# Performance work log

Measured on AMD Instinct MI355X. Metric: run time of the kernel, lower is better.

## Reference

```python
import jax, jax.numpy as jnp
import numpy as np

D_MODEL = 1024
NUM_HEADS = 16
D_K = D_MODEL // NUM_HEADS


def setup_inputs() -> dict:
    key = jax.random.key(0)
    ks = jax.random.split(key, 5)
    s = 1.0 / np.sqrt(D_MODEL)  # xavier-ish scale
    x = jax.random.normal(ks[0], (2, 2048, D_MODEL), dtype=jnp.float32)
    Wq = jax.random.normal(ks[1], (D_MODEL, D_MODEL), dtype=jnp.float32) * s
    Wk = jax.random.normal(ks[2], (D_MODEL, D_MODEL), dtype=jnp.float32) * s
    Wv = jax.random.normal(ks[3], (D_MODEL, D_MODEL), dtype=jnp.float32) * s
    Wo = jax.random.normal(ks[4], (D_MODEL, D_MODEL), dtype=jnp.float32) * s
    z = jnp.zeros((D_MODEL,), dtype=jnp.float32)
    return {"x": x, "Wq": Wq, "bq": z, "Wk": Wk, "bk": z, "Wv": Wv, "bv": z, "Wo": Wo, "bo": z}


def reference(x, Wq, bq, Wk, bk, Wv, bv, Wo, bo):
    B, S, _ = x.shape
    # torch Linear: y = x @ W.T + b
    def split_heads(t):
        return t.reshape(B, S, NUM_HEADS, D_K).transpose(0, 2, 1, 3)  # [B,H,S,Dk]
    q = split_heads(x @ Wq.T + bq)
    k = split_heads(x @ Wk.T + bk)
    v = split_heads(x @ Wv.T + bv)
    scores = jnp.einsum('bhqd,bhkd->bhqk', q, k) / jnp.sqrt(jnp.float32(D_K))
    attn = jax.nn.softmax(scores, axis=-1)
    out = jnp.einsum('bhqk,bhkd->bhqd', attn, v)  # [B,H,S,Dk]
    out = out.transpose(0, 2, 1, 3).reshape(B, S, D_MODEL)
    return out @ Wo.T + bo
```

## Files before the change

kernel.cpp:

```cpp
#include <hip/hip_runtime.h>
#include <hip/hip_bf16.h>
#include <type_traits>


typedef __attribute__((ext_vector_type(4))) float f32x4;
typedef __attribute__((ext_vector_type(16))) float f32x16;
typedef __attribute__((ext_vector_type(8))) short s16x8;
typedef __attribute__((ext_vector_type(4))) unsigned int u32x4;

#define GLDS16(g, l)                                                       \
  __builtin_amdgcn_global_load_lds(                                        \
      (const __attribute__((address_space(1))) unsigned int*)(g),          \
      (__attribute__((address_space(3))) unsigned int*)(l), 16, 0, 0)

#define SCALE_Q 0.18033688011112042f

__device__ __forceinline__ unsigned short f2bf(float f) {
  unsigned int u = __builtin_bit_cast(unsigned int, f);
  u += 0x7fffu + ((u >> 16) & 1u);
  return (unsigned short)(u >> 16);
}

__device__ __forceinline__ unsigned int cvtpk_bf16(float lo, float hi) {
  unsigned int r;
  asm("v_cvt_pk_bf16_f32 %0, %1, %2" : "=v"(r) : "v"(lo), "v"(hi));
  return r;
}

__device__ __forceinline__ float fexp2(float x) {
  return __builtin_amdgcn_exp2f(x);
}

__global__ void cvt_f32_bf16(const float* __restrict__ in,
                             unsigned short* __restrict__ out, int n,
                             float scale) {
  int i = (blockIdx.x * blockDim.x + threadIdx.x) * 4;
  if (i < n) {
    float4 v = *reinterpret_cast<const float4*>(in + i);
    ushort4 o;
    o.x = f2bf(v.x * scale); o.y = f2bf(v.y * scale);
    o.z = f2bf(v.z * scale); o.w = f2bf(v.w * scale);
    *reinterpret_cast<ushort4*>(out + i) = o;
  }
}

__global__ void concat3(const float* __restrict__ a, const float* __restrict__ b,
                        const float* __restrict__ c, float* __restrict__ out) {
  int i = blockIdx.x * blockDim.x + threadIdx.x;
  const float* src = (i < 1024) ? a : ((i < 2048) ? b : c);
  float s = (i < 1024) ? SCALE_Q : 1.0f;
  out[i] = src[i & 1023] * s;
}

template <typename CT>
__global__ __launch_bounds__(256, 2) void gemm_bt(
    const unsigned short* __restrict__ A, const unsigned short* __restrict__ B,
    CT* __restrict__ C, int M, int N, int K, const float* __restrict__ bias) {
  __shared__ unsigned short As[128 * 32];
  __shared__ unsigned short Bs[128 * 32];
  const int tid = threadIdx.x;
  const int wv = tid >> 6, lane = tid & 63;
  const int g = lane >> 4, c16 = lane & 15;
  const int wm = wv >> 1, wn = wv & 1;
  const int bm = blockIdx.y, bn = blockIdx.x;

  const unsigned short* Ab = A + (size_t)bm * 128 * K;
  const unsigned short* Bb = B + (size_t)bn * 128 * K;

  f32x4 acc[4][4] = {};

  for (int k0 = 0; k0 < K; k0 += 32) {
    __syncthreads();
#pragma unroll
    for (int r = 0; r < 2; ++r) {
      int i = r * 256 + tid;
      int row = i >> 2, col = (i & 3) * 8;
      GLDS16(Ab + (size_t)row * K + k0 + col, &As[i * 8]);
    }
#pragma unroll
    for (int r = 0; r < 2; ++r) {
      int i = r * 256 + tid;
      int row = i >> 2, col = (i & 3) * 8;
      GLDS16(Bb + (size_t)row * K + k0 + col, &Bs[i * 8]);
    }
    __syncthreads();

    s16x8 af[4], bfv[4];
#pragma unroll
    for (int m = 0; m < 4; ++m)
      af[m] = *(const s16x8*)&As[(wm * 64 + m * 16 + c16) * 32 + g * 8];
#pragma unroll
    for (int n = 0; n < 4; ++n)
      bfv[n] = *(const s16x8*)&Bs[(wn * 64 + n * 16 + c16) * 32 + g * 8];
#pragma unroll
    for (int m = 0; m < 4; ++m)
#pragma unroll
      for (int n = 0; n < 4; ++n)
        acc[m][n] = __builtin_amdgcn_mfma_f32_16x16x32_bf16(af[m], bfv[n],
                                                            acc[m][n], 0, 0, 0);
  }

#pragma unroll
  for (int m = 0; m < 4; ++m) {
#pragma unroll
    for (int n = 0; n < 4; ++n) {
      int col = bn * 128 + wn * 64 + n * 16 + c16;
      float bb = bias ? bias[col] : 0.f;
#pragma unroll
      for (int j = 0; j < 4; ++j) {
        int row = bm * 128 + wm * 64 + m * 16 + g * 4 + j;
        float v = acc[m][n][j] + bb;
        if constexpr (std::is_same<CT, float>::value)
          C[(size_t)row * N + col] = v;
        else
          C[(size_t)row * N + col] = f2bf(v);
      }
    }
  }
}

__global__ void transpose_v(const unsigned short* __restrict__ qkv,
                            unsigned short* __restrict__ vt) {
  __shared__ unsigned short T[64 * 80];
  const int tid = threadIdx.x;
  const int st = blockIdx.x, bh = blockIdx.y;
  const int b = bh >> 4, h = bh & 15;
  const int s0 = st * 64;

  int srow = tid >> 2, d0 = (tid & 3) * 16;
  const unsigned short* src =
      qkv + (size_t)(b * 2048 + s0 + srow) * 3072 + 2048 + h * 64 + d0;
  s16x8 v0 = *(const s16x8*)(src);
  s16x8 v1 = *(const s16x8*)(src + 8);
  *(s16x8*)&T[srow * 80 + d0] = v0;
  *(s16x8*)&T[srow * 80 + d0 + 8] = v1;
  __syncthreads();

  int drow = tid >> 2, sl = (tid & 3) * 16;
  s16x8 o0, o1;
#pragma unroll
  for (int j = 0; j < 8; ++j) o0[j] = (short)T[(sl + j) * 80 + drow];
#pragma unroll
  for (int j = 0; j < 8; ++j) o1[j] = (short)T[(sl + 8 + j) * 80 + drow];
  unsigned short* dst = vt + (size_t)(bh * 64 + drow) * 2048 + s0 + sl;
  *(s16x8*)dst = o0;
  *(s16x8*)(dst + 8) = o1;
}

__global__ __launch_bounds__(1024) void flash_attn(
    const unsigned short* __restrict__ qkv, const unsigned short* __restrict__ vt,
    unsigned short* __restrict__ attn) {
  __shared__ __align__(16) char smem[68608];
  unsigned short* KsB = (unsigned short*)smem;
  unsigned short* VTsB = (unsigned short*)(smem + 32768);
  float* MoB = (float*)smem;
  float* MlB = (float*)(smem + 66560);

  const int tid = threadIdx.x;
  const int wv = tid >> 6, lane = tid & 63;
  const int half = wv >> 3, w8 = wv & 7;
  const int col = lane & 31, hi = lane >> 5;
  const int qt = blockIdx.x, bh = blockIdx.y;
  const int b = bh >> 4, h = bh & 15;
  const int qrow0 = qt * 256 + w8 * 32;

  const int stid = tid & 511;
  const int srow = stid >> 3, scs = stid & 7;
  const int sqc = scs ^ (srow & 7);
  const int kbase = half * 1024;
  const unsigned short* kgsrc =
      qkv + (size_t)(b * 2048 + kbase + srow) * 3072 + 1024 + h * 64 + sqc * 8;
  const unsigned short* vgsrc =
      vt + (size_t)(bh * 64 + srow) * 2048 + kbase + sqc * 8;

  s16x8 qb[4];
#pragma unroll
  for (int ds = 0; ds < 4; ++ds)
    qb[ds] = *(const s16x8*)(qkv + (size_t)(b * 2048 + qrow0 + col) * 3072 +
                             h * 64 + ds * 16 + hi * 8);

  s16x8 onev;
#pragma unroll
  for (int j = 0; j < 8; ++j) onev[j] = (short)0x3F80;

  f32x16 o[2] = {};
  f32x16 lacc = {};

  GLDS16(kgsrc, &KsB[half * 8192 + stid * 8]);
  GLDS16(vgsrc, &VTsB[half * 8192 + stid * 8]);
  __syncthreads();

  for (int kt = 0; kt < 16; ++kt) {
    const int cur = kt & 1;
    const unsigned short* Kc = &KsB[(half * 2 + cur) * 4096];
    const unsigned short* Vc = &VTsB[(half * 2 + cur) * 4096];
    if (kt < 15) {
      GLDS16(kgsrc + (size_t)(kt + 1) * 64 * 3072,
             &KsB[(half * 2 + (cur ^ 1)) * 4096 + stid * 8]);
      GLDS16(vgsrc + (kt + 1) * 64,
             &VTsB[(half * 2 + (cur ^ 1)) * 4096 + stid * 8]);
    }

    f32x16 st[2];
    __builtin_amdgcn_s_setprio(1);
#pragma unroll
    for (int kb = 0; kb < 2; ++kb) {
      f32x16 a = {};
#pragma unroll
      for (int ds = 0; ds < 4; ++ds) {
        int row = kb * 32 + col;
        int cs = ds * 2 + hi;
        s16x8 ka = *(const s16x8*)&Kc[row * 64 + (cs ^ (row & 7)) * 8];
        a = __builtin_amdgcn_mfma_f32_32x32x16_bf16(ka, qb[ds], a, 0, 0, 0);
      }
      st[kb] = a;
    }
    __builtin_amdgcn_s_setprio(0);

#pragma unroll
    for (int kb = 0; kb < 2; ++kb)
#pragma unroll
      for (int r = 0; r < 16; ++r) st[kb][r] = fexp2(st[kb][r]);

#pragma unroll
    for (int kb = 0; kb < 2; ++kb) {
#pragma unroll
      for (int hf = 0; hf < 2; ++hf) {
        const int p0 = hf * 8;
        unsigned int a0 = cvtpk_bf16(st[kb][p0 + 0], st[kb][p0 + 1]);
        unsigned int b0 = cvtpk_bf16(st[kb][p0 + 4], st[kb][p0 + 5]);
        unsigned int a1 = cvtpk_bf16(st[kb][p0 + 2], st[kb][p0 + 3]);
        unsigned int b1 = cvtpk_bf16(st[kb][p0 + 6], st[kb][p0 + 7]);
        asm("v_permlane32_swap_b32 %0, %1" : "+v"(a0), "+v"(b0));
        asm("v_permlane32_swap_b32 %0, %1" : "+v"(a1), "+v"(b1));
        u32x4 pw;
        pw[0] = a0; pw[1] = a1; pw[2] = b0; pw[3] = b1;
        const s16x8 pa = __builtin_bit_cast(s16x8, pw);
        const int ks = kb * 2 + hf;
        __builtin_amdgcn_s_setprio(1);
#pragma unroll
        for (int n = 0; n < 2; ++n) {
          int row = n * 32 + col;
          int cs = ks * 2 + hi;
          s16x8 vb = *(const s16x8*)&Vc[row * 64 + (cs ^ (row & 7)) * 8];
          o[n] = __builtin_amdgcn_mfma_f32_32x32x16_bf16(pa, vb, o[n], 0, 0, 0);
        }
        lacc = __builtin_amdgcn_mfma_f32_32x32x16_bf16(pa, onev, lacc, 0, 0, 0);
        __builtin_amdgcn_s_setprio(0);
      }
    }
    __syncthreads();
  }

  if (half == 1) {
#pragma unroll
    for (int r = 0; r < 16; ++r) {
      int qd = (r & 3) + 8 * (r >> 2) + 4 * hi;
      MoB[(w8 * 32 + qd) * 65 + col] = o[0][r];
      MoB[(w8 * 32 + qd) * 65 + 32 + col] = o[1][r];
      if (col == 0) MlB[w8 * 32 + qd] = lacc[r];
    }
  }
  __syncthreads();
  if (half == 0) {
#pragma unroll
    for (int r = 0; r < 16; ++r) {
      int qd = (r & 3) + 8 * (r >> 2) + 4 * hi;
      float linv = 1.f / (lacc[r] + MlB[w8 * 32 + qd]);
      float v0 = (o[0][r] + MoB[(w8 * 32 + qd) * 65 + col]) * linv;
      float v1 = (o[1][r] + MoB[(w8 * 32 + qd) * 65 + 32 + col]) * linv;
      size_t base = (size_t)(b * 2048 + qrow0 + qd) * 1024 + h * 64;
      attn[base + col] = f2bf(v0);
      attn[base + 32 + col] = f2bf(v1);
    }
  }
}

extern "C" void kernel_launch(void* const* d_in, const int* in_sizes, int n_in,
                              void* d_out, int out_size, void* d_ws, size_t ws_size,
                              hipStream_t stream) {
  const float* x  = (const float*)d_in[0];
  const float* Wq = (const float*)d_in[1];
  const float* bq = (const float*)d_in[2];
  const float* Wk = (const float*)d_in[3];
  const float* bk = (const float*)d_in[4];
  const float* Wv = (const float*)d_in[5];
  const float* bv = (const float*)d_in[6];
  const float* Wo = (const float*)d_in[7];
  const float* bo = (const float*)d_in[8];
  float* out = (float*)d_out;

  char* ws = (char*)d_ws;
  const size_t MB = 1024 * 1024;
  unsigned short* xb   = (unsigned short*)(ws + 0);
  unsigned short* attn = (unsigned short*)(ws + 0);
  unsigned short* wob  = (unsigned short*)(ws + 8 * MB);
  unsigned short* wcat = (unsigned short*)(ws + 10 * MB);
  unsigned short* vt   = (unsigned short*)(ws + 10 * MB);
  unsigned short* qkv  = (unsigned short*)(ws + 18 * MB);
  float* bcat          = (float*)(ws + 42 * MB);

  cvt_f32_bf16<<<4096, 256, 0, stream>>>(x, xb, 4 * 1024 * 1024, 1.0f);
  cvt_f32_bf16<<<1024, 256, 0, stream>>>(Wq, wcat, 1024 * 1024, SCALE_Q);
  cvt_f32_bf16<<<1024, 256, 0, stream>>>(Wk, wcat + 1024 * 1024, 1024 * 1024, 1.0f);
  cvt_f32_bf16<<<1024, 256, 0, stream>>>(Wv, wcat + 2 * 1024 * 1024, 1024 * 1024, 1.0f);
  cvt_f32_bf16<<<1024, 256, 0, stream>>>(Wo, wob, 1024 * 1024, 1.0f);
  concat3<<<12, 256, 0, stream>>>(bq, bk, bv, bcat);

  gemm_bt<unsigned short><<<dim3(24, 32), 256, 0, stream>>>(
      xb, wcat, qkv, 4096, 3072, 1024, bcat);

  transpose_v<<<dim3(32, 32), 256, 0, stream>>>(qkv, vt);

  flash_attn<<<dim3(8, 32), 1024, 0, stream>>>(qkv, vt, attn);

  gemm_bt<float><<<dim3(8, 32), 256, 0, stream>>>(
      attn, wob, out, 4096, 1024, 1024, bo);
}
```

Baseline: 128.6 us.

## Shrink attention blocks to 128 queries and fuse conversion kernels

Flash attention now uses 512-thread blocks covering 128 query rows instead of 1024 threads covering 256, which doubles the grid to 512 blocks for better CU coverage. Each thread now issues two async global-to-LDS loads per K and V tile, so the same 64-row tiles are still staged. The cost is that each block's K/V loads are shared by half as many queries, so total K/V traffic doubles. Separately, the five fp32-to-bf16 conversion launches are merged into one kernel that picks its source by global index, removing launch overhead.

New measurement: 126.0 us. 1.02x faster.

```diff
diff --git a/kernel.cpp b/kernel.cpp
--- a/kernel.cpp
+++ b/kernel.cpp
@@ -31,17 +31,33 @@
   return __builtin_amdgcn_exp2f(x);
 }
 
-__global__ void cvt_f32_bf16(const float* __restrict__ in,
-                             unsigned short* __restrict__ out, int n,
-                             float scale) {
-  int i = (blockIdx.x * blockDim.x + threadIdx.x) * 4;
-  if (i < n) {
-    float4 v = *reinterpret_cast<const float4*>(in + i);
-    ushort4 o;
-    o.x = f2bf(v.x * scale); o.y = f2bf(v.y * scale);
-    o.z = f2bf(v.z * scale); o.w = f2bf(v.w * scale);
-    *reinterpret_cast<ushort4*>(out + i) = o;
-  }
+__global__ void cvt_all(const float* __restrict__ x, const float* __restrict__ Wq,
+                        const float* __restrict__ Wk, const float* __restrict__ Wv,
+                        const float* __restrict__ Wo,
+                        unsigned short* __restrict__ xb,
+                        unsigned short* __restrict__ wcat,
+                        unsigned short* __restrict__ wob) {
+  int g = blockIdx.x * blockDim.x + threadIdx.x;
+  const float* in;
+  unsigned short* out;
+  int off;
+  float scale = 1.0f;
+  if (g < 1048576) {
+    in = x; out = xb; off = g;
+  } else if (g < 1310720) {
+    in = Wq; out = wcat; off = g - 1048576; scale = SCALE_Q;
+  } else if (g < 1572864) {
+    in = Wk; out = wcat + 1048576; off = g - 1310720;
+  } else if (g < 1835008) {
+    in = Wv; out = wcat + 2097152; off = g - 1572864;
+  } else {
+    in = Wo; out = wob; off = g - 1835008;
+  }
+  float4 v = *reinterpret_cast<const float4*>(in + off * 4);
+  ushort4 o;
+  o.x = f2bf(v.x * scale); o.y = f2bf(v.y * scale);
+  o.z = f2bf(v.z * scale); o.w = f2bf(v.w * scale);
+  *reinterpret_cast<ushort4*>(out + off * 4) = o;
 }
 
 __global__ void concat3(const float* __restrict__ a, const float* __restrict__ b,
@@ -147,7 +163,7 @@
   *(s16x8*)(dst + 8) = o1;
 }
 
-__global__ __launch_bounds__(1024) void flash_attn(
+__global__ __launch_bounds__(512) void flash_attn(
     const unsigned short* __restrict__ qkv, const unsigned short* __restrict__ vt,
     unsigned short* __restrict__ attn) {
   __shared__ __align__(16) char smem[68608];
@@ -158,20 +174,25 @@
 
   const int tid = threadIdx.x;
   const int wv = tid >> 6, lane = tid & 63;
-  const int half = wv >> 3, w8 = wv & 7;
+  const int half = wv >> 2, w4 = wv & 3;
   const int col = lane & 31, hi = lane >> 5;
   const int qt = blockIdx.x, bh = blockIdx.y;
   const int b = bh >> 4, h = bh & 15;
-  const int qrow0 = qt * 256 + w8 * 32;
-
-  const int stid = tid & 511;
-  const int srow = stid >> 3, scs = stid & 7;
-  const int sqc = scs ^ (srow & 7);
+  const int qrow0 = qt * 128 + w4 * 32;
+
+  const int stid = tid & 255;
   const int kbase = half * 1024;
-  const unsigned short* kgsrc =
-      qkv + (size_t)(b * 2048 + kbase + srow) * 3072 + 1024 + h * 64 + sqc * 8;
-  const unsigned short* vgsrc =
-      vt + (size_t)(bh * 64 + srow) * 2048 + kbase + sqc * 8;
+  const int idx0 = stid, idx1 = stid + 256;
+  const int sr0 = idx0 >> 3, sc0 = (idx0 & 7) ^ (sr0 & 7);
+  const int sr1 = idx1 >> 3, sc1 = (idx1 & 7) ^ (sr1 & 7);
+  const unsigned short* kg0 =
+      qkv + (size_t)(b * 2048 + kbase + sr0) * 3072 + 1024 + h * 64 + sc0 * 8;
+  const unsigned short* kg1 =
+      qkv + (size_t)(b * 2048 + kbase + sr1) * 3072 + 1024 + h * 64 + sc1 * 8;
+  const unsigned short* vg0 =
+      vt + (size_t)(bh * 64 + sr0) * 2048 + kbase + sc0 * 8;
+  const unsigned short* vg1 =
+      vt + (size_t)(bh * 64 + sr1) * 2048 + kbase + sc1 * 8;
 
   s16x8 qb[4];
 #pragma unroll
@@ -186,8 +207,14 @@
   f32x16 o[2] = {};
   f32x16 lacc = {};
 
-  GLDS16(kgsrc, &KsB[half * 8192 + stid * 8]);
-  GLDS16(vgsrc, &VTsB[half * 8192 + stid * 8]);
+  {
+    unsigned short* kd = &KsB[half * 8192];
+    unsigned short* vd = &VTsB[half * 8192];
+    GLDS16(kg0, &kd[idx0 * 8]);
+    GLDS16(kg1, &kd[idx1 * 8]);
+    GLDS16(vg0, &vd[idx0 * 8]);
+    GLDS16(vg1, &vd[idx1 * 8]);
+  }
   __syncthreads();
 
   for (int kt = 0; kt < 16; ++kt) {
@@ -195,10 +222,13 @@
     const unsigned short* Kc = &KsB[(half * 2 + cur) * 4096];
     const unsigned short* Vc = &VTsB[(half * 2 + cur) * 4096];
     if (kt < 15) {
-      GLDS16(kgsrc + (size_t)(kt + 1) * 64 * 3072,
-             &KsB[(half * 2 + (cur ^ 1)) * 4096 + stid * 8]);
-      GLDS16(vgsrc + (kt + 1) * 64,
-             &VTsB[(half * 2 + (cur ^ 1)) * 4096 + stid * 8]);
+      unsigned short* kd = &KsB[(half * 2 + (cur ^ 1)) * 4096];
+      unsigned short* vd = &VTsB[(half * 2 + (cur ^ 1)) * 4096];
+      const size_t ko = (size_t)(kt + 1) * 64 * 3072;
+      GLDS16(kg0 + ko, &kd[idx0 * 8]);
+      GLDS16(kg1 + ko, &kd[idx1 * 8]);
+      GLDS16(vg0 + (kt + 1) * 64, &vd[idx0 * 8]);
+      GLDS16(vg1 + (kt + 1) * 64, &vd[idx1 * 8]);
     }
 
     f32x16 st[2];
@@ -256,9 +286,9 @@
 #pragma unroll
     for (int r = 0; r < 16; ++r) {
       int qd = (r & 3) + 8 * (r >> 2) + 4 * hi;
-      MoB[(w8 * 32 + qd) * 65 + col] = o[0][r];
-      MoB[(w8 * 32 + qd) * 65 + 32 + col] = o[1][r];
-      if (col == 0) MlB[w8 * 32 + qd] = lacc[r];
+      MoB[(w4 * 32 + qd) * 65 + col] = o[0][r];
+      MoB[(w4 * 32 + qd) * 65 + 32 + col] = o[1][r];
+      if (col == 0) MlB[w4 * 32 + qd] = lacc[r];
     }
   }
   __syncthreads();
@@ -266,9 +296,9 @@
 #pragma unroll
     for (int r = 0; r < 16; ++r) {
       int qd = (r & 3) + 8 * (r >> 2) + 4 * hi;
-      float linv = 1.f / (lacc[r] + MlB[w8 * 32 + qd]);
-      float v0 = (o[0][r] + MoB[(w8 * 32 + qd) * 65 + col]) * linv;
-      float v1 = (o[1][r] + MoB[(w8 * 32 + qd) * 65 + 32 + col]) * linv;
+      float linv = 1.f / (lacc[r] + MlB[w4 * 32 + qd]);
+      float v0 = (o[0][r] + MoB[(w4 * 32 + qd) * 65 + col]) * linv;
+      float v1 = (o[1][r] + MoB[(w4 * 32 + qd) * 65 + 32 + col]) * linv;
       size_t base = (size_t)(b * 2048 + qrow0 + qd) * 1024 + h * 64;
       attn[base + col] = f2bf(v0);
       attn[base + 32 + col] = f2bf(v1);
@@ -300,11 +330,7 @@
   unsigned short* qkv  = (unsigned short*)(ws + 18 * MB);
   float* bcat          = (float*)(ws + 42 * MB);
 
-  cvt_f32_bf16<<<4096, 256, 0, stream>>>(x, xb, 4 * 1024 * 1024, 1.0f);
-  cvt_f32_bf16<<<1024, 256, 0, stream>>>(Wq, wcat, 1024 * 1024, SCALE_Q);
-  cvt_f32_bf16<<<1024, 256, 0, stream>>>(Wk, wcat + 1024 * 1024, 1024 * 1024, 1.0f);
-  cvt_f32_bf16<<<1024, 256, 0, stream>>>(Wv, wcat + 2 * 1024 * 1024, 1024 * 1024, 1.0f);
-  cvt_f32_bf16<<<1024, 256, 0, stream>>>(Wo, wob, 1024 * 1024, 1.0f);
+  cvt_all<<<8192, 256, 0, stream>>>(x, Wq, Wk, Wv, Wo, xb, wcat, wob);
   concat3<<<12, 256, 0, stream>>>(bq, bk, bv, bcat);
 
   gemm_bt<unsigned short><<<dim3(24, 32), 256, 0, stream>>>(
@@ -312,7 +338,7 @@
 
   transpose_v<<<dim3(32, 32), 256, 0, stream>>>(qkv, vt);
 
-  flash_attn<<<dim3(8, 32), 1024, 0, stream>>>(qkv, vt, attn);
+  flash_attn<<<dim3(16, 32), 512, 0, stream>>>(qkv, vt, attn);
 
   gemm_bt<float><<<dim3(8, 32), 256, 0, stream>>>(
       attn, wob, out, 4096, 1024, 1024, bo);
```
